# Performance work log

Measured on AMD Instinct MI355X. Metric: run time of the kernel, lower is better.

The kernel has to match this reference:

```python
import jax, jax.numpy as jnp
import numpy as np

B, S, HID = 1, 2048, 4096
N_HEADS, N_KV, HEAD_DIM = 32, 8, 128
N_REP = N_HEADS // N_KV
ROPE_THETA = 10000.0
NEG_INF = -1e9


def setup_inputs() -> dict:
    key = jax.random.key(0)
    ks = jax.random.split(key, 5)
    hidden_states = jax.random.normal(ks[0], (B, S, HID), dtype=jnp.float32)
    Wq = jax.random.normal(ks[1], (HID, N_HEADS * HEAD_DIM), dtype=jnp.float32) * 0.02
    Wk = jax.random.normal(ks[2], (HID, N_KV * HEAD_DIM), dtype=jnp.float32) * 0.02
    Wv = jax.random.normal(ks[3], (HID, N_KV * HEAD_DIM), dtype=jnp.float32) * 0.02
    Wo = jax.random.normal(ks[4], (N_HEADS * HEAD_DIM, HID), dtype=jnp.float32) * 0.02
    # causal additive mask [B, 1, S, S]
    causal = jnp.tril(jnp.ones((S, S), dtype=bool))
    attention_mask = jnp.where(causal, 0.0, NEG_INF).astype(jnp.float32)[None, None]
    position_ids = jnp.broadcast_to(jnp.arange(S, dtype=jnp.int32)[None], (B, S))
    return {
        "hidden_states": hidden_states, "Wq": Wq, "Wk": Wk, "Wv": Wv, "Wo": Wo,
        "attention_mask": attention_mask, "position_ids": position_ids,
    }


def _rotate_half(x):
    half = x.shape[-1] // 2
    return jnp.concatenate([-x[..., half:], x[..., :half]], axis=-1)


def _rope_tables(position_ids):
    # inv_freq: [head_dim/2]
    inv_freq = 1.0 / (ROPE_THETA ** (jnp.arange(0, HEAD_DIM, 2, dtype=jnp.float32) / HEAD_DIM))
    # freqs: [B, S, head_dim/2]
    freqs = position_ids.astype(jnp.float32)[..., None] * inv_freq
    emb = jnp.concatenate([freqs, freqs], axis=-1)  # [B, S, head_dim]
    # [B, 1, S, head_dim] to broadcast over heads
    return jnp.cos(emb)[:, None], jnp.sin(emb)[:, None]


def reference(hidden_states, Wq, Wk, Wv, Wo, attention_mask, position_ids):
    b, s, _ = hidden_states.shape
    # projections -> [B, H, S, D]
    q = (hidden_states @ Wq).reshape(b, s, N_HEADS, HEAD_DIM).transpose(0, 2, 1, 3)
    k = (hidden_states @ Wk).reshape(b, s, N_KV, HEAD_DIM).transpose(0, 2, 1, 3)
    v = (hidden_states @ Wv).reshape(b, s, N_KV, HEAD_DIM).transpose(0, 2, 1, 3)
    cos, sin = _rope_tables(position_ids)
    q = q * cos + _rotate_half(q) * sin
    k = k * cos + _rotate_half(k) * sin
    # GQA repeat_kv (repeat_interleave over head dim)
    k = jnp.repeat(k, N_REP, axis=1)
    v = jnp.repeat(v, N_REP, axis=1)
    scores = jnp.einsum("bhqd,bhkd->bhqk", q, k) / jnp.sqrt(jnp.float32(HEAD_DIM))
    scores = scores + attention_mask
    probs = jax.nn.softmax(scores.astype(jnp.float32), axis=-1).astype(q.dtype)
    attn = jnp.einsum("bhqk,bhkd->bhqd", probs, v)
    attn = attn.transpose(0, 2, 1, 3).reshape(b, s, N_HEADS * HEAD_DIM)
    return attn @ Wo
```

## Files before the change

### kernel.cpp

```cpp
#include <hip/hip_runtime.h>
#include <hip/hip_bf16.h>

#define S_LEN 2048
#define HIDDEN 4096
#define NH 32
#define NKV 8
#define HD 128
#define NQKV 6144

typedef __bf16 bf16_t;
typedef __bf16 bf16x8 __attribute__((ext_vector_type(8)));
typedef __bf16 bf16x4 __attribute__((ext_vector_type(4)));
typedef float f32x4 __attribute__((ext_vector_type(4)));

typedef __attribute__((address_space(1))) void gvoid;
typedef __attribute__((address_space(3))) void lvoid;

__device__ __forceinline__ void gload_lds16(const void* g, void* l) {
    __builtin_amdgcn_global_load_lds((gvoid*)g, (lvoid*)l, 16, 0, 0);
}

__device__ __forceinline__ float fast_exp2(float x) {
    return __builtin_amdgcn_exp2f(x);
}

__global__ void cast_bf16_kernel(const float* __restrict__ in, bf16_t* __restrict__ out, int n4) {
    int stride = gridDim.x * blockDim.x;
    for (int idx = blockIdx.x * blockDim.x + threadIdx.x; idx < n4; idx += stride) {
        float4 v = ((const float4*)in)[idx];
        bf16x4 o;
        o.x = (bf16_t)v.x; o.y = (bf16_t)v.y; o.z = (bf16_t)v.z; o.w = (bf16_t)v.w;
        ((bf16x4*)out)[idx] = o;
    }
}

__global__ __launch_bounds__(256) void transpose_cast_kernel(const float* __restrict__ in,
                                                             bf16_t* __restrict__ out,
                                                             int ldin, int ldout) {
    __shared__ float t[32][33];
    int c0 = blockIdx.x * 32, r0 = blockIdx.y * 32;
    int tx = threadIdx.x, ty = threadIdx.y;
#pragma unroll
    for (int i = 0; i < 4; ++i)
        t[ty + i * 8][tx] = in[(size_t)(r0 + ty + i * 8) * ldin + c0 + tx];
    __syncthreads();
#pragma unroll
    for (int i = 0; i < 4; ++i)
        out[(size_t)(c0 + ty + i * 8) * ldout + r0 + tx] = (bf16_t)t[tx][ty + i * 8];
}

__global__ __launch_bounds__(256) void transpose_bf16_kernel(const bf16_t* __restrict__ in,
                                                             bf16_t* __restrict__ out,
                                                             int ldin, int ldout) {
    __shared__ float t[32][33];
    int c0 = blockIdx.x * 32, r0 = blockIdx.y * 32;
    int tx = threadIdx.x, ty = threadIdx.y;
#pragma unroll
    for (int i = 0; i < 4; ++i)
        t[ty + i * 8][tx] = (float)in[(size_t)(r0 + ty + i * 8) * ldin + c0 + tx];
    __syncthreads();
#pragma unroll
    for (int i = 0; i < 4; ++i)
        out[(size_t)(c0 + ty + i * 8) * ldout + r0 + tx] = (bf16_t)t[tx][ty + i * 8];
}

template<typename OutT>
__global__ __launch_bounds__(512, 2) void gemm_ring_kernel(const bf16_t* __restrict__ A,
                                                           const bf16_t* __restrict__ Bt,
                                                           OutT* __restrict__ C,
                                                           int M, int N, int K) {
    __shared__ bf16_t As[3][128 * 32];
    __shared__ bf16_t Bs[3][256 * 32];
    const int tid = threadIdx.x;
    const int lane = tid & 63, w = tid >> 6;
    const int wm = w >> 2, wn = w & 3;
    const int g = lane >> 4, c16 = lane & 15;
    const int srow = lane >> 2;
    const int scg = ((lane & 3) ^ ((lane >> 3) & 3)) * 8;
    const int rdc = (g ^ ((c16 >> 1) & 3)) * 8;

    const int nbm = M / 128;
    const int cpx = gridDim.x >> 3;
    const int bid = blockIdx.x;
    const int swz = (bid & 7) * cpx + (bid >> 3);
    const int bm = swz % nbm, bn = swz / nbm;

    const bf16_t* Ab = A + (size_t)(bm * 128) * K;
    const bf16_t* Bb = Bt + (size_t)(bn * 256) * K;

    auto stage = [&](int slot, int kt) {
        const bf16_t* Ak = Ab + (size_t)kt * 32;
        const bf16_t* Bk = Bb + (size_t)kt * 32;
        {
            int rb = 16 * w;
            gload_lds16(Ak + (size_t)(rb + srow) * K + scg, &As[slot][rb * 32]);
        }
#pragma unroll
        for (int j = 0; j < 2; ++j) {
            int rb = 32 * w + 16 * j;
            gload_lds16(Bk + (size_t)(rb + srow) * K + scg, &Bs[slot][rb * 32]);
        }
    };

    f32x4 acc[4][4];
#pragma unroll
    for (int i = 0; i < 4; ++i)
#pragma unroll
        for (int j = 0; j < 4; ++j)
            acc[i][j] = (f32x4){0.f, 0.f, 0.f, 0.f};

    const int NT = K / 32;
    stage(0, 0);
    stage(1, 1);

    int slot = 0, slot2 = 2;
    for (int t = 0; t < NT; ++t) {
        asm volatile("s_waitcnt vmcnt(3)" ::: "memory");
        __builtin_amdgcn_s_barrier();
        __builtin_amdgcn_sched_barrier(0);
        __builtin_amdgcn_s_setprio(1);

        bf16x8 af[4], bf[4];
#pragma unroll
        for (int i = 0; i < 4; ++i) {
            int arow = wm * 64 + i * 16 + c16;
            af[i] = *(const bf16x8*)&As[slot][arow * 32 + rdc];
            int brow = wn * 64 + i * 16 + c16;
            bf[i] = *(const bf16x8*)&Bs[slot][brow * 32 + rdc];
        }
        int nk = t + 2;
        if (nk >= NT) nk -= NT;
        stage(slot2, nk);

#pragma unroll
        for (int i = 0; i < 4; ++i)
#pragma unroll
            for (int j = 0; j < 4; ++j)
                acc[i][j] = __builtin_amdgcn_mfma_f32_16x16x32_bf16(af[i], bf[j], acc[i][j], 0, 0, 0);
        __builtin_amdgcn_s_setprio(0);

        slot = (slot + 1) % 3;
        slot2 = (slot2 + 1) % 3;
    }

#pragma unroll
    for (int mi = 0; mi < 4; ++mi)
#pragma unroll
        for (int ni = 0; ni < 4; ++ni) {
            int col = bn * 256 + wn * 64 + ni * 16 + c16;
#pragma unroll
            for (int r = 0; r < 4; ++r) {
                int row = bm * 128 + wm * 64 + mi * 16 + g * 4 + r;
                C[(size_t)row * N + col] = (OutT)acc[mi][ni][r];
            }
        }
}

__global__ void rope_kernel(const bf16_t* __restrict__ in, bf16_t* __restrict__ out,
                            const int* __restrict__ pos, int H, int ld, float scale) {
    int idx = blockIdx.x * blockDim.x + threadIdx.x;
    int total = S_LEN * H * 64;
    if (idx >= total) return;
    int d = idx & 63;
    int h = (idx >> 6) % H;
    int s = idx / (64 * H);
    const bf16_t* base = in + (size_t)s * ld + h * HD;
    float x0 = (float)base[d], x1 = (float)base[d + 64];
    float p = (float)pos[s];
    float invf = fast_exp2(-0.20762050593046935f * (float)d);
    float f = p * invf;
    float sn, cs;
    __sincosf(f, &sn, &cs);
    float o0 = (x0 * cs - x1 * sn) * scale;
    float o1 = (x1 * cs + x0 * sn) * scale;
    bf16_t* ob = out + ((size_t)h * S_LEN + s) * HD;
    ob[d] = (bf16_t)o0;
    ob[d + 64] = (bf16_t)o1;
}

#define PLD 72
__global__ __launch_bounds__(256) void attn_kernel(const bf16_t* __restrict__ Q,
                                                   const bf16_t* __restrict__ K,
                                                   const bf16_t* __restrict__ Vt,
                                                   bf16_t* __restrict__ O) {
    __shared__ bf16_t Ks[2][64 * 128];
    __shared__ bf16_t Vs[2][128 * 64];
    __shared__ bf16_t Pl[4][16 * PLD];
    const int tid = threadIdx.x;
    const int lane = tid & 63, w = tid >> 6;
    const int bid = blockIdx.x;
    const int h = bid & 31;
    const int x = bid >> 5;
    const int kv = h >> 2;
    const int qb = x * 64 + w * 16;
    const int g = lane >> 4, c16 = lane & 15;
    const int c7 = c16 & 7;
    const bf16_t* Qh = Q + (size_t)h * S_LEN * HD;
    const bf16_t* Kh = K + (size_t)kv * S_LEN * HD;
    const bf16_t* Vh = Vt + (size_t)kv * HD * S_LEN;
    bf16_t* P = Pl[w];

    auto stage = [&](int buf, int kb) {
        bf16_t* Kd = Ks[buf];
        bf16_t* Vd = Vs[buf];
#pragma unroll
        for (int j = 0; j < 4; ++j) {
            int i = w * 4 + j;
            {
                int row = 4 * i + (lane >> 4);
                int sc = (lane & 15) ^ (row & 7);
                gload_lds16(Kh + (size_t)(kb + row) * HD + sc * 8, Kd + i * 512);
            }
            {
                int row = 8 * i + (lane >> 3);
                int sc = (lane & 7) ^ ((lane >> 3) & 7);
                gload_lds16(Vh + (size_t)row * S_LEN + kb + sc * 8, Vd + i * 512);
            }
        }
    };

    bf16x8 qf[4];
#pragma unroll
    for (int c = 0; c < 4; ++c)
        qf[c] = *(const bf16x8*)(Qh + (size_t)(qb + c16) * HD + c * 32 + g * 8);

    f32x4 acc_o[8];
#pragma unroll
    for (int dt = 0; dt < 8; ++dt) acc_o[dt] = (f32x4){0.f, 0.f, 0.f, 0.f};
    float m[4] = {-1e30f, -1e30f, -1e30f, -1e30f};
    float l[4] = {0.f, 0.f, 0.f, 0.f};

    const int nkt = x + 1;
    stage(0, 0);
    __syncthreads();
    int cur = 0;

    for (int kt = 0; kt < nkt; ++kt) {
        if (kt + 1 < nkt) stage(cur ^ 1, (kt + 1) * 64);
        const int kb = kt * 64;
        const bf16_t* Kb = Ks[cur];
        const bf16_t* Vb = Vs[cur];
        const bool diag = (kt == nkt - 1);

        f32x4 sacc[4];
#pragma unroll
        for (int t = 0; t < 4; ++t) sacc[t] = (f32x4){0.f, 0.f, 0.f, 0.f};
#pragma unroll
        for (int t = 0; t < 4; ++t) {
            const bf16_t* krow = Kb + (t * 16 + c16) * 128;
#pragma unroll
            for (int cc = 0; cc < 4; ++cc) {
                bf16x8 kf = *(const bf16x8*)(krow + (((cc * 4 + g) ^ c7) * 8));
                sacc[t] = __builtin_amdgcn_mfma_f32_16x16x32_bf16(qf[cc], kf, sacc[t], 0, 0, 0);
            }
        }
        float p[4][4], alpha[4];
#pragma unroll
        for (int r = 0; r < 4; ++r) {
            int qq = qb + g * 4 + r;
            float s[4];
#pragma unroll
            for (int t = 0; t < 4; ++t)
                s[t] = (!diag || (kb + t * 16 + c16 <= qq)) ? sacc[t][r] : -1e30f;
            float mx = fmaxf(fmaxf(s[0], s[1]), fmaxf(s[2], s[3]));
            mx = fmaxf(mx, __shfl_xor(mx, 1));
            mx = fmaxf(mx, __shfl_xor(mx, 2));
            mx = fmaxf(mx, __shfl_xor(mx, 4));
            mx = fmaxf(mx, __shfl_xor(mx, 8));
            float mn = fmaxf(m[r], mx);
            alpha[r] = fast_exp2(m[r] - mn);
            m[r] = mn;
            float rs = 0.f;
#pragma unroll
            for (int t = 0; t < 4; ++t) {
                p[t][r] = fast_exp2(s[t] - mn);
                rs += p[t][r];
            }
            rs += __shfl_xor(rs, 1);
            rs += __shfl_xor(rs, 2);
            rs += __shfl_xor(rs, 4);
            rs += __shfl_xor(rs, 8);
            l[r] = l[r] * alpha[r] + rs;
        }
#pragma unroll
        for (int dt = 0; dt < 8; ++dt)
#pragma unroll
            for (int r = 0; r < 4; ++r) acc_o[dt][r] *= alpha[r];
#pragma unroll
        for (int t = 0; t < 4; ++t)
#pragma unroll
            for (int r = 0; r < 4; ++r)
                P[(g * 4 + r) * PLD + t * 16 + c16] = (bf16_t)p[t][r];
        bf16x8 pf[2];
        pf[0] = *(const bf16x8*)(P + c16 * PLD + g * 8);
        pf[1] = *(const bf16x8*)(P + c16 * PLD + 32 + g * 8);
#pragma unroll
        for (int dt = 0; dt < 8; ++dt) {
            const bf16_t* vrow = Vb + (dt * 16 + c16) * 64;
            bf16x8 vf0 = *(const bf16x8*)(vrow + ((g ^ c7) * 8));
            bf16x8 vf1 = *(const bf16x8*)(vrow + (((4 + g) ^ c7) * 8));
            acc_o[dt] = __builtin_amdgcn_mfma_f32_16x16x32_bf16(pf[0], vf0, acc_o[dt], 0, 0, 0);
            acc_o[dt] = __builtin_amdgcn_mfma_f32_16x16x32_bf16(pf[1], vf1, acc_o[dt], 0, 0, 0);
        }
        __syncthreads();
        cur ^= 1;
    }
    float inv_l[4];
#pragma unroll
    for (int r = 0; r < 4; ++r) inv_l[r] = 1.f / l[r];
#pragma unroll
    for (int dt = 0; dt < 8; ++dt)
#pragma unroll
        for (int r = 0; r < 4; ++r)
            O[(size_t)(qb + g * 4 + r) * HIDDEN + h * HD + dt * 16 + c16] =
                (bf16_t)(acc_o[dt][r] * inv_l[r]);
}

extern "C" void kernel_launch(void* const* d_in, const int* in_sizes, int n_in,
                              void* d_out, int out_size, void* d_ws, size_t ws_size,
                              hipStream_t stream) {
    const float* hs = (const float*)d_in[0];
    const float* Wq = (const float*)d_in[1];
    const float* Wk = (const float*)d_in[2];
    const float* Wv = (const float*)d_in[3];
    const float* Wo = (const float*)d_in[4];
    const int* pos = (const int*)d_in[6];
    float* out = (float*)d_out;

    char* ws = (char*)d_ws;
    size_t off = 0;
    auto alloc = [&](size_t bytes) -> void* {
        void* p = ws + off;
        off += (bytes + 255) & ~(size_t)255;
        return p;
    };
    bf16_t* hB    = (bf16_t*)alloc((size_t)S_LEN * HIDDEN * 2);
    bf16_t* WqkvT = (bf16_t*)alloc((size_t)NQKV * HIDDEN * 2);
    bf16_t* WoT   = (bf16_t*)alloc((size_t)HIDDEN * HIDDEN * 2);
    bf16_t* QKV   = (bf16_t*)alloc((size_t)S_LEN * NQKV * 2);
    bf16_t* Qr    = (bf16_t*)alloc((size_t)NH * S_LEN * HD * 2);
    bf16_t* Kr    = (bf16_t*)alloc((size_t)NKV * S_LEN * HD * 2);
    bf16_t* Vt    = (bf16_t*)alloc((size_t)NKV * HD * S_LEN * 2);
    bf16_t* Oat   = (bf16_t*)alloc((size_t)S_LEN * HIDDEN * 2);

    dim3 tb(32, 8);
    cast_bf16_kernel<<<2048, 256, 0, stream>>>(hs, hB, S_LEN * HIDDEN / 4);
    transpose_cast_kernel<<<dim3(HIDDEN / 32, HIDDEN / 32), tb, 0, stream>>>(Wq, WqkvT, HIDDEN, HIDDEN);
    transpose_cast_kernel<<<dim3(1024 / 32, HIDDEN / 32), tb, 0, stream>>>(Wk, WqkvT + (size_t)4096 * HIDDEN, 1024, HIDDEN);
    transpose_cast_kernel<<<dim3(1024 / 32, HIDDEN / 32), tb, 0, stream>>>(Wv, WqkvT + (size_t)5120 * HIDDEN, 1024, HIDDEN);
    transpose_cast_kernel<<<dim3(HIDDEN / 32, HIDDEN / 32), tb, 0, stream>>>(Wo, WoT, HIDDEN, HIDDEN);
    gemm_ring_kernel<bf16_t><<<(S_LEN / 128) * (NQKV / 256), 512, 0, stream>>>(hB, WqkvT, QKV, S_LEN, NQKV, HIDDEN);
    rope_kernel<<<(S_LEN * NH * 64 + 255) / 256, 256, 0, stream>>>(QKV, Qr, pos, NH, NQKV, 0.1275174310f);
    rope_kernel<<<(S_LEN * NKV * 64 + 255) / 256, 256, 0, stream>>>(QKV + 4096, Kr, pos, NKV, NQKV, 1.0f);
    transpose_bf16_kernel<<<dim3(1024 / 32, S_LEN / 32), tb, 0, stream>>>(QKV + 5120, Vt, NQKV, S_LEN);
    attn_kernel<<<1024, 256, 0, stream>>>(Qr, Kr, Vt, Oat);
    gemm_ring_kernel<float><<<(S_LEN / 128) * (HIDDEN / 256), 512, 0, stream>>>(Oat, WoT, out, S_LEN, HIDDEN, HIDDEN);
}
```

Measured before the change: 384.6 us.

## Load V directly to registers, lazy rescale, compute row sums via MFMA

```diff
diff --git a/kernel.cpp b/kernel.cpp
--- a/kernel.cpp
+++ b/kernel.cpp
@@ -179,12 +179,11 @@
 }
 
 #define PLD 72
-__global__ __launch_bounds__(256) void attn_kernel(const bf16_t* __restrict__ Q,
-                                                   const bf16_t* __restrict__ K,
-                                                   const bf16_t* __restrict__ Vt,
-                                                   bf16_t* __restrict__ O) {
+__global__ __launch_bounds__(256, 3) void attn_kernel(const bf16_t* __restrict__ Q,
+                                                      const bf16_t* __restrict__ K,
+                                                      const bf16_t* __restrict__ Vt,
+                                                      bf16_t* __restrict__ O) {
     __shared__ bf16_t Ks[2][64 * 128];
-    __shared__ bf16_t Vs[2][128 * 64];
     __shared__ bf16_t Pl[4][16 * PLD];
     const int tid = threadIdx.x;
     const int lane = tid & 63, w = tid >> 6;
@@ -200,22 +199,14 @@
     const bf16_t* Vh = Vt + (size_t)kv * HD * S_LEN;
     bf16_t* P = Pl[w];
 
-    auto stage = [&](int buf, int kb) {
+    auto stageK = [&](int buf, int kb) {
         bf16_t* Kd = Ks[buf];
-        bf16_t* Vd = Vs[buf];
 #pragma unroll
         for (int j = 0; j < 4; ++j) {
             int i = w * 4 + j;
-            {
-                int row = 4 * i + (lane >> 4);
-                int sc = (lane & 15) ^ (row & 7);
-                gload_lds16(Kh + (size_t)(kb + row) * HD + sc * 8, Kd + i * 512);
-            }
-            {
-                int row = 8 * i + (lane >> 3);
-                int sc = (lane & 7) ^ ((lane >> 3) & 7);
-                gload_lds16(Vh + (size_t)row * S_LEN + kb + sc * 8, Vd + i * 512);
-            }
+            int row = 4 * i + (lane >> 4);
+            int sc = (lane & 15) ^ (row & 7);
+            gload_lds16(Kh + (size_t)(kb + row) * HD + sc * 8, Kd + i * 512);
         }
     };
 
@@ -224,22 +215,32 @@
     for (int c = 0; c < 4; ++c)
         qf[c] = *(const bf16x8*)(Qh + (size_t)(qb + c16) * HD + c * 32 + g * 8);
 
+    bf16x8 ones;
+#pragma unroll
+    for (int j = 0; j < 8; ++j) ones[j] = (bf16_t)1.0f;
+
     f32x4 acc_o[8];
 #pragma unroll
     for (int dt = 0; dt < 8; ++dt) acc_o[dt] = (f32x4){0.f, 0.f, 0.f, 0.f};
+    f32x4 acc_l = (f32x4){0.f, 0.f, 0.f, 0.f};
     float m[4] = {-1e30f, -1e30f, -1e30f, -1e30f};
-    float l[4] = {0.f, 0.f, 0.f, 0.f};
 
     const int nkt = x + 1;
-    stage(0, 0);
+    stageK(0, 0);
     __syncthreads();
     int cur = 0;
 
     for (int kt = 0; kt < nkt; ++kt) {
-        if (kt + 1 < nkt) stage(cur ^ 1, (kt + 1) * 64);
         const int kb = kt * 64;
+        if (kt + 1 < nkt) stageK(cur ^ 1, (kt + 1) * 64);
+        bf16x8 v0[4][2];
+#pragma unroll
+        for (int dt = 0; dt < 4; ++dt) {
+            const bf16_t* vrow = Vh + (size_t)(dt * 16 + c16) * S_LEN + kb;
+            v0[dt][0] = *(const bf16x8*)(vrow + g * 8);
+            v0[dt][1] = *(const bf16x8*)(vrow + 32 + g * 8);
+        }
         const bf16_t* Kb = Ks[cur];
-        const bf16_t* Vb = Vs[cur];
         const bool diag = (kt == nkt - 1);
 
         f32x4 sacc[4];
@@ -254,38 +255,42 @@
                 sacc[t] = __builtin_amdgcn_mfma_f32_16x16x32_bf16(qf[cc], kf, sacc[t], 0, 0, 0);
             }
         }
-        float p[4][4], alpha[4];
+        float p[4][4], mxr[4];
 #pragma unroll
         for (int r = 0; r < 4; ++r) {
             int qq = qb + g * 4 + r;
-            float s[4];
-#pragma unroll
-            for (int t = 0; t < 4; ++t)
-                s[t] = (!diag || (kb + t * 16 + c16 <= qq)) ? sacc[t][r] : -1e30f;
-            float mx = fmaxf(fmaxf(s[0], s[1]), fmaxf(s[2], s[3]));
+#pragma unroll
+            for (int t = 0; t < 4; ++t) {
+                float sv = sacc[t][r];
+                if (diag && (kb + t * 16 + c16 > qq)) sv = -1e30f;
+                p[t][r] = sv;
+            }
+            float mx = fmaxf(fmaxf(p[0][r], p[1][r]), fmaxf(p[2][r], p[3][r]));
             mx = fmaxf(mx, __shfl_xor(mx, 1));
             mx = fmaxf(mx, __shfl_xor(mx, 2));
             mx = fmaxf(mx, __shfl_xor(mx, 4));
             mx = fmaxf(mx, __shfl_xor(mx, 8));
-            float mn = fmaxf(m[r], mx);
-            alpha[r] = fast_exp2(m[r] - mn);
-            m[r] = mn;
-            float rs = 0.f;
-#pragma unroll
-            for (int t = 0; t < 4; ++t) {
-                p[t][r] = fast_exp2(s[t] - mn);
-                rs += p[t][r];
+            mxr[r] = mx;
+        }
+        bool resc = false;
+#pragma unroll
+        for (int r = 0; r < 4; ++r) resc = resc || (mxr[r] > m[r] + 8.f);
+        if (__any(resc)) {
+#pragma unroll
+            for (int r = 0; r < 4; ++r) {
+                float mn = fmaxf(m[r], mxr[r]);
+                float al = fast_exp2(m[r] - mn);
+                m[r] = mn;
+                acc_l[r] *= al;
+#pragma unroll
+                for (int dt = 0; dt < 8; ++dt) acc_o[dt][r] *= al;
             }
-            rs += __shfl_xor(rs, 1);
-            rs += __shfl_xor(rs, 2);
-            rs += __shfl_xor(rs, 4);
-            rs += __shfl_xor(rs, 8);
-            l[r] = l[r] * alpha[r] + rs;
-        }
-#pragma unroll
-        for (int dt = 0; dt < 8; ++dt)
-#pragma unroll
-            for (int r = 0; r < 4; ++r) acc_o[dt][r] *= alpha[r];
+        }
+#pragma unroll
+        for (int r = 0; r < 4; ++r)
+#pragma unroll
+            for (int t = 0; t < 4; ++t)
+                p[t][r] = fast_exp2(p[t][r] - m[r]);
 #pragma unroll
         for (int t = 0; t < 4; ++t)
 #pragma unroll
@@ -294,20 +299,31 @@
         bf16x8 pf[2];
         pf[0] = *(const bf16x8*)(P + c16 * PLD + g * 8);
         pf[1] = *(const bf16x8*)(P + c16 * PLD + 32 + g * 8);
-#pragma unroll
-        for (int dt = 0; dt < 8; ++dt) {
-            const bf16_t* vrow = Vb + (dt * 16 + c16) * 64;
-            bf16x8 vf0 = *(const bf16x8*)(vrow + ((g ^ c7) * 8));
-            bf16x8 vf1 = *(const bf16x8*)(vrow + (((4 + g) ^ c7) * 8));
-            acc_o[dt] = __builtin_amdgcn_mfma_f32_16x16x32_bf16(pf[0], vf0, acc_o[dt], 0, 0, 0);
-            acc_o[dt] = __builtin_amdgcn_mfma_f32_16x16x32_bf16(pf[1], vf1, acc_o[dt], 0, 0, 0);
+        bf16x8 v1[4][2];
+#pragma unroll
+        for (int dt = 0; dt < 4; ++dt) {
+            const bf16_t* vrow = Vh + (size_t)((dt + 4) * 16 + c16) * S_LEN + kb;
+            v1[dt][0] = *(const bf16x8*)(vrow + g * 8);
+            v1[dt][1] = *(const bf16x8*)(vrow + 32 + g * 8);
+        }
+        acc_l = __builtin_amdgcn_mfma_f32_16x16x32_bf16(pf[0], ones, acc_l, 0, 0, 0);
+        acc_l = __builtin_amdgcn_mfma_f32_16x16x32_bf16(pf[1], ones, acc_l, 0, 0, 0);
+#pragma unroll
+        for (int dt = 0; dt < 4; ++dt) {
+            acc_o[dt] = __builtin_amdgcn_mfma_f32_16x16x32_bf16(pf[0], v0[dt][0], acc_o[dt], 0, 0, 0);
+            acc_o[dt] = __builtin_amdgcn_mfma_f32_16x16x32_bf16(pf[1], v0[dt][1], acc_o[dt], 0, 0, 0);
+        }
+#pragma unroll
+        for (int dt = 0; dt < 4; ++dt) {
+            acc_o[dt + 4] = __builtin_amdgcn_mfma_f32_16x16x32_bf16(pf[0], v1[dt][0], acc_o[dt + 4], 0, 0, 0);
+            acc_o[dt + 4] = __builtin_amdgcn_mfma_f32_16x16x32_bf16(pf[1], v1[dt][1], acc_o[dt + 4], 0, 0, 0);
         }
         __syncthreads();
         cur ^= 1;
     }
     float inv_l[4];
 #pragma unroll
-    for (int r = 0; r < 4; ++r) inv_l[r] = 1.f / l[r];
+    for (int r = 0; r < 4; ++r) inv_l[r] = 1.f / acc_l[r];
 #pragma unroll
     for (int dt = 0; dt < 8; ++dt)
 #pragma unroll
```

New measurement: 440.4 us. 14.5% more time.
